# Performance work log

Measured on AMD Instinct MI355X. Metric: run time of the kernel, lower is better.

## Reference

```python
import jax, jax.numpy as jnp
import numpy as np

B, T, C = 1, 2048, 1024
H, HKV, DH, WIN = 16, 4, 64, 128
EPS = 1e-5


def rotate_half(x):
    x1, x2 = jnp.split(x, 2, axis=-1)
    return jnp.concatenate((-x2, x1), axis=-1)


def setup_inputs() -> dict:
    key = jax.random.key(0)
    ks = jax.random.split(key, 8)
    s = 0.02
    return {
        "x": jax.random.normal(ks[0], (B, T, C), dtype=jnp.float32),
        "Wq": jax.random.normal(ks[1], (C, H * DH), dtype=jnp.float32) * s,
        "Wk": jax.random.normal(ks[2], (C, HKV * DH), dtype=jnp.float32) * s,
        "Wv": jax.random.normal(ks[3], (C, HKV * DH), dtype=jnp.float32) * s,
        "Wc": jax.random.normal(ks[4], (C, C), dtype=jnp.float32) * s,
        "Wg": jax.random.normal(ks[5], (C, H), dtype=jnp.float32) * s,
        "bg": jax.random.normal(ks[6], (H,), dtype=jnp.float32) * s,
        "rms_w": jnp.ones((C,), dtype=jnp.float32),
    }


def reference(x, Wq, Wk, Wv, Wc, Wg, bg, rms_w):
    n_rep = H // HKV
    # projections -> [B, heads, T, DH]
    q = (x @ Wq).reshape(B, T, H, DH).transpose(0, 2, 1, 3)
    k = (x @ Wk).reshape(B, T, HKV, DH).transpose(0, 2, 1, 3)
    v = (x @ Wv).reshape(B, T, HKV, DH).transpose(0, 2, 1, 3)
    # rotary embedding (freqs duplicated across the two halves)
    inv_freq = 1.0 / (10000.0 ** (jnp.arange(0, DH, 2, dtype=jnp.float32) / DH))
    freqs = jnp.arange(T, dtype=jnp.float32)[:, None] * inv_freq[None, :]
    emb = jnp.concatenate((freqs, freqs), axis=-1)  # [T, DH]
    cos, sin = jnp.cos(emb)[None, None], jnp.sin(emb)[None, None]
    q = q * cos + rotate_half(q) * sin
    k = k * cos + rotate_half(k) * sin
    # GQA: repeat kv heads (contiguous repeat matches torch expand+reshape)
    k = jnp.repeat(k, n_rep, axis=1)
    v = jnp.repeat(v, n_rep, axis=1)
    # gated decay
    gate_logits = (x @ Wg + bg).reshape(B, T, H, 1).transpose(0, 2, 1, 3)  # [B,H,T,1]
    log_alpha = jax.nn.log_sigmoid(gate_logits)
    log_in_scale = jax.nn.log_sigmoid(-gate_logits)
    k_scaled = k * jnp.exp(log_in_scale)
    la_cum = jnp.cumsum(log_alpha, axis=2)                  # [B,H,T,1]
    log_decay = la_cum - jnp.swapaxes(la_cum, 2, 3)         # [B,H,T,T]
    causal = jnp.triu(jnp.ones((T, T), dtype=bool), k=1)
    decay = jnp.exp(jnp.where(causal, -jnp.inf, log_decay))
    scores = jnp.einsum('bhtd,bhsd->bhts', q, k_scaled)
    y_global = jnp.einsum('bhts,bhsd->bhtd', scores * decay, v)
    nb = T // WIN
    qb = q.reshape(B, H, nb, WIN, DH)
    kb = k.reshape(B, H, nb, WIN, DH)
    vb = v.reshape(B, H, nb, WIN, DH)
    att = jnp.einsum('bhnqd,bhnkd->bhnqk', qb, kb) / jnp.sqrt(jnp.float32(DH))
    wmask = jnp.triu(jnp.ones((WIN, WIN), dtype=bool), k=1)
    att = jax.nn.softmax(jnp.where(wmask, -jnp.inf, att), axis=-1)
    y_local = jnp.einsum('bhnqk,bhnkd->bhnqd', att, vb).reshape(B, H, T, DH)
    # fuse, RMSNorm, output projection
    y = (y_global + y_local).transpose(0, 2, 1, 3).reshape(B, T, C)
    y = y * jax.lax.rsqrt(jnp.mean(y * y, axis=-1, keepdims=True) + EPS) * rms_w
    return y @ Wc
```

## Files before the change

kernel.cpp:

```cpp
#include <hip/hip_runtime.h>
#include <hip/hip_bf16.h>


typedef __attribute__((ext_vector_type(8))) short bf16x8;
typedef __attribute__((ext_vector_type(4))) float f32x4;

#define MFMA16(a, b, c) __builtin_amdgcn_mfma_f32_16x16x32_bf16(a, b, c, 0, 0, 0)
#define LN10000_OVER_32 0.28782313662425575f

__device__ __forceinline__ short f2b(float f) {
  __hip_bfloat16 h = __float2bfloat16(f);
  return *reinterpret_cast<short*>(&h);
}
__device__ __forceinline__ float b2f(short s) {
  return __uint_as_float(((unsigned)(unsigned short)s) << 16);
}
__device__ __forceinline__ void gload16(const void* g, void* l) {
  __builtin_amdgcn_global_load_lds(
      (const __attribute__((address_space(1))) void*)g,
      (__attribute__((address_space(3))) void*)l, 16, 0, 0);
}

__device__ __forceinline__ void transpose_cvt_body(
    const float* __restrict__ src, short* __restrict__ dst, int R, int C,
    int bx, int by, float* ts , const float* __restrict__ sw) {
  int c0 = bx * 32, r0 = by * 32;
  int tr = threadIdx.x >> 3, tc = (threadIdx.x & 7) * 4;
  float4 v = *(const float4*)&src[(size_t)(r0 + tr) * C + c0 + tc];
  ts[tr * 33 + tc] = v.x;
  ts[tr * 33 + tc + 1] = v.y;
  ts[tr * 33 + tc + 2] = v.z;
  ts[tr * 33 + tc + 3] = v.w;
  __syncthreads();
  alignas(8) short o[4];
#pragma unroll
  for (int i = 0; i < 4; ++i) {
    float m = sw ? sw[r0 + tc + i] : 1.0f;
    o[i] = f2b(ts[(tc + i) * 33 + tr] * m);
  }
  *(uint2*)&dst[(size_t)(c0 + tr) * R + r0 + tc] = *(uint2*)o;
}

__global__ __launch_bounds__(256) void prep_fused(
    const float* __restrict__ x, const float* __restrict__ Wq,
    const float* __restrict__ Wk, const float* __restrict__ Wv,
    const float* __restrict__ Wc, const float* __restrict__ Wg,
    const float* __restrict__ bg, const float* __restrict__ rmsw,
    short* __restrict__ xb, short* __restrict__ wqkvT,
    short* __restrict__ wcT, float* __restrict__ g, float* __restrict__ rs) {
  __shared__ float ts[32 * 33];
  const int j = blockIdx.x;
  const int tid = threadIdx.x;
  if (j < 2048) {
    const int t = j;
    const int h = tid & 15, chunk = tid >> 4;
    const float* xr = x + (size_t)t * 1024 + chunk * 64;
    const float* wg = Wg + (size_t)chunk * 64 * 16 + h;
    float acc = 0.f;
#pragma unroll
    for (int c = 0; c < 64; c += 4) {
      float4 xv = *(const float4*)(xr + c);
      acc = fmaf(xv.x, wg[(c + 0) * 16], acc);
      acc = fmaf(xv.y, wg[(c + 1) * 16], acc);
      acc = fmaf(xv.z, wg[(c + 2) * 16], acc);
      acc = fmaf(xv.w, wg[(c + 3) * 16], acc);
    }
    ts[chunk * 16 + h] = acc;
    __syncthreads();
    if (tid < 16) {
      float s = bg[tid];
#pragma unroll
      for (int i = 0; i < 16; ++i) s += ts[i * 16 + tid];
      g[t * 16 + tid] = s;
    }
  } else if (j < 3072) {
    int i = ((j - 2048) * 256 + tid) * 8;
    float4 a = *(const float4*)(x + i);
    float4 b = *(const float4*)(x + i + 4);
    alignas(16) short o[8] = {f2b(a.x), f2b(a.y), f2b(a.z), f2b(a.w),
                              f2b(b.x), f2b(b.y), f2b(b.z), f2b(b.w)};
    *(float4*)(xb + i) = *(float4*)o;
  } else if (j < 4096) {
    int jj = j - 3072;
    transpose_cvt_body(Wq, wqkvT, 1024, 1024, jj & 31, jj >> 5, ts, nullptr);
  } else if (j < 4352) {
    int jj = j - 4096;
    transpose_cvt_body(Wk, wqkvT + 1024 * 1024, 1024, 256, jj & 7, jj >> 3, ts,
                       nullptr);
  } else if (j < 4608) {
    int jj = j - 4352;
    transpose_cvt_body(Wv, wqkvT + 1280 * 1024, 1024, 256, jj & 7, jj >> 3, ts,
                       nullptr);
  } else if (j < 5632) {
    int jj = j - 4608;
    transpose_cvt_body(Wc, wcT, 1024, 1024, jj & 31, jj >> 5, ts, rmsw);
  } else {
    int i4 = ((j - 5632) * 256 + tid) * 4;
    float4 z = {0.f, 0.f, 0.f, 0.f};
    *(float4*)(rs + i4) = z;
  }
}

__global__ __launch_bounds__(256) void qkv_gemm_fused(
    const short* __restrict__ A, const short* __restrict__ Bt,
    short* __restrict__ qkvb, short* __restrict__ vtb,
    short* __restrict__ ktb, const float* __restrict__ g,
    float* __restrict__ lac, float* __restrict__ insc) {
  __shared__ short As[128 * 64];
  __shared__ short Bs[64 * 64];
  __shared__ float part[256];
  const int id = blockIdx.x;
  const int tid = threadIdx.x;
  if (id >= 384) {
    const int h = id - 384;
    float vals[8];
    float local = 0.f;
#pragma unroll
    for (int i = 0; i < 8; ++i) {
      int t = tid * 8 + i;
      float gv = g[t * 16 + h];
      float la = (gv > 0.f) ? -log1pf(expf(-gv)) : (gv - log1pf(expf(gv)));
      insc[h * 2048 + t] = 1.f / (1.f + expf(gv));
      vals[i] = la;
      local += la;
    }
    part[tid] = local;
    __syncthreads();
    for (int off = 1; off < 256; off <<= 1) {
      float add = (tid >= off) ? part[tid - off] : 0.f;
      __syncthreads();
      part[tid] += add;
      __syncthreads();
    }
    float run = (tid > 0) ? part[tid - 1] : 0.f;
#pragma unroll
    for (int i = 0; i < 8; ++i) {
      run += vals[i];
      lac[h * 2048 + tid * 8 + i] = run;
    }
    return;
  }
  const int lane = tid & 63, wid = tid >> 6;
  const int l15 = lane & 15, lq = lane >> 4;
  const int jlin = id >> 3;
  const int by = (id & 7) + 8 * (jlin / 24);
  const int bx = jlin % 24;
  const int m0 = by * 128, n0 = bx * 64;
  const int K = 1024;
  const int srow = lane >> 3;
  const int sc16 = (lane & 7) ^ srow;
  f32x4 acc[2][4];
#pragma unroll
  for (int mt = 0; mt < 2; ++mt)
#pragma unroll
    for (int nt = 0; nt < 4; ++nt) acc[mt][nt] = {0.f, 0.f, 0.f, 0.f};
  for (int kt = 0; kt < K; kt += 64) {
    __syncthreads();
#pragma unroll
    for (int i = 0; i < 4; ++i) {
      int jj = wid * 4 + i;
      int row = jj * 8 + srow;
      gload16(A + (size_t)(m0 + row) * K + kt + sc16 * 8, &As[jj * 512]);
    }
#pragma unroll
    for (int i = 0; i < 2; ++i) {
      int jj = wid * 2 + i;
      int row = jj * 8 + srow;
      gload16(Bt + (size_t)(n0 + row) * K + kt + sc16 * 8, &Bs[jj * 512]);
    }
    __syncthreads();
    bf16x8 af[2][2], bfr[4][2];
#pragma unroll
    for (int ks = 0; ks < 2; ++ks) {
      int c16 = ks * 4 + lq;
#pragma unroll
      for (int mt = 0; mt < 2; ++mt) {
        int ar = wid * 32 + mt * 16 + l15;
        af[mt][ks] = *(const bf16x8*)&As[(ar * 8 + (c16 ^ (ar & 7))) * 8];
      }
#pragma unroll
      for (int nt = 0; nt < 4; ++nt) {
        int br = nt * 16 + l15;
        bfr[nt][ks] = *(const bf16x8*)&Bs[(br * 8 + (c16 ^ (br & 7))) * 8];
      }
    }
#pragma unroll
    for (int ks = 0; ks < 2; ++ks)
#pragma unroll
      for (int mt = 0; mt < 2; ++mt)
#pragma unroll
        for (int nt = 0; nt < 4; ++nt)
          acc[mt][nt] = MFMA16(af[mt][ks], bfr[nt][ks], acc[mt][nt]);
  }
  if (bx >= 20) {
#pragma unroll
    for (int mt = 0; mt < 2; ++mt) {
      int row0 = m0 + wid * 32 + mt * 16 + lq * 4;
#pragma unroll
      for (int nt = 0; nt < 4; ++nt) {
        int vcol = (n0 - 1280) + nt * 16 + l15;
        alignas(8) short o4[4];
#pragma unroll
        for (int r = 0; r < 4; ++r) o4[r] = f2b(acc[mt][nt][r]);
        *(uint2*)&vtb[(size_t)vcol * 2048 + row0] = *(uint2*)o4;
      }
    }
    return;
  }
  const bool isk = (bx >= 16);
#pragma unroll
  for (int mt = 0; mt < 2; ++mt) {
    int row0 = m0 + wid * 32 + mt * 16 + lq * 4;
#pragma unroll
    for (int nt = 0; nt < 2; ++nt) {
      int d = nt * 16 + l15;
      float ivf = __expf(-LN10000_OVER_32 * (float)d);
      alignas(8) short oa[4], ob[4];
#pragma unroll
      for (int r = 0; r < 4; ++r) {
        int row_g = row0 + r;
        float th = (float)row_g * ivf;
        float cs = cosf(th), sn = sinf(th);
        float a = acc[mt][nt][r], b = acc[mt][nt + 2][r];
        oa[r] = f2b(a * cs - b * sn);
        ob[r] = f2b(b * cs + a * sn);
        qkvb[(size_t)row_g * 1536 + n0 + d] = oa[r];
        qkvb[(size_t)row_g * 1536 + n0 + d + 32] = ob[r];
      }
      if (isk) {
        int dk = n0 - 1024 + d;
        *(uint2*)&ktb[(size_t)dk * 2048 + row0] = *(uint2*)oa;
        *(uint2*)&ktb[(size_t)(dk + 32) * 2048 + row0] = *(uint2*)ob;
      }
    }
  }
}

__global__ __launch_bounds__(256) void chunk_state(
    const short* __restrict__ vtb, const short* __restrict__ ktb,
    const float* __restrict__ lac, const float* __restrict__ insc,
    float* __restrict__ Bmat) {
  __shared__ short Ks[64 * 64], Vts[64 * 64];
  __shared__ float lacs[64], inss[64], gvals[64];
  const int tid = threadIdx.x, lane = tid & 63, wid = tid >> 6;
  const int l15 = lane & 15, lq = lane >> 4;
  const int h = blockIdx.y, kh = h >> 2, c = blockIdx.x;
  const int srow = lane >> 3;
  const int sc16 = (lane & 7) ^ srow;
#pragma unroll
  for (int i = 0; i < 2; ++i) {
    int jj = wid * 2 + i;
    int row = jj * 8 + srow;
    gload16(ktb + (size_t)(kh * 64 + row) * 2048 + c * 64 + sc16 * 8,
            &Ks[jj * 512]);
    gload16(vtb + (size_t)(kh * 64 + row) * 2048 + c * 64 + sc16 * 8,
            &Vts[jj * 512]);
  }
  if (tid < 64) {
    lacs[tid] = lac[h * 2048 + c * 64 + tid];
    inss[tid] = insc[h * 2048 + c * 64 + tid];
  }
  __syncthreads();
  if (tid < 64)
    gvals[tid] = __expf(fminf(lacs[63] - lacs[tid], 0.f)) * inss[tid];
  __syncthreads();
  const int er = wid * 16 + l15;
  bf16x8 av[2];
#pragma unroll
  for (int ks = 0; ks < 2; ++ks) {
    int c16 = ks * 4 + lq;
    bf16x8 raw = *(const bf16x8*)&Vts[(er * 8 + (c16 ^ (er & 7))) * 8];
    float4 g0 = *(const float4*)&gvals[c16 * 8];
    float4 g1 = *(const float4*)&gvals[c16 * 8 + 4];
    float gv[8] = {g0.x, g0.y, g0.z, g0.w, g1.x, g1.y, g1.z, g1.w};
    bf16x8 sc;
#pragma unroll
    for (int jx = 0; jx < 8; ++jx) sc[jx] = f2b(b2f(raw[jx]) * gv[jx]);
    av[ks] = sc;
  }
  f32x4 acc[4];
#pragma unroll
  for (int nt = 0; nt < 4; ++nt) acc[nt] = {0.f, 0.f, 0.f, 0.f};
#pragma unroll
  for (int ks = 0; ks < 2; ++ks) {
    int c16 = ks * 4 + lq;
#pragma unroll
    for (int nt = 0; nt < 4; ++nt) {
      int dr = nt * 16 + l15;
      bf16x8 bk = *(const bf16x8*)&Ks[(dr * 8 + (c16 ^ (dr & 7))) * 8];
      acc[nt] = MFMA16(av[ks], bk, acc[nt]);
    }
  }
  float* Bout = Bmat + (size_t)(h * 32 + c) * 4096;
#pragma unroll
  for (int nt = 0; nt < 4; ++nt)
#pragma unroll
    for (int r = 0; r < 4; ++r) {
      int e = wid * 16 + lq * 4 + r;
      Bout[e * 64 + nt * 16 + l15] = acc[nt][r];
    }
}

__global__ __launch_bounds__(256) void scan_kernel(
    const float* __restrict__ Bmat, const float* __restrict__ lac,
    short* __restrict__ St) {
  const int h = blockIdx.x, sl = blockIdx.y, tid = threadIdx.x;
  __shared__ float lacE[32];
  if (tid < 32) lacE[tid] = lac[h * 2048 + tid * 64 + 63];
  __syncthreads();
  const int base = sl * 512 + tid * 2;
  float S0 = 0.f, S1 = 0.f;
  *(unsigned*)&St[(size_t)(h * 32) * 4096 + base] = 0u;
  float2 p = *(const float2*)(Bmat + (size_t)(h * 32) * 4096 + base);
  for (int c = 1; c < 32; ++c) {
    float2 n = p;
    if (c < 31) n = *(const float2*)(Bmat + (size_t)(h * 32 + c) * 4096 + base);
    float a = (c >= 2) ? __expf(fminf(lacE[c - 1] - lacE[c - 2], 0.f)) : 0.f;
    S0 = fmaf(a, S0, p.x);
    S1 = fmaf(a, S1, p.y);
    unsigned pack = (unsigned)(unsigned short)f2b(S0) |
                    ((unsigned)(unsigned short)f2b(S1) << 16);
    *(unsigned*)&St[(size_t)(h * 32 + c) * 4096 + base] = pack;
    p = n;
  }
}

__global__ __launch_bounds__(256) void fused_attn(
    const short* __restrict__ qkv, const short* __restrict__ vtb,
    const short* __restrict__ St, const float* __restrict__ lac,
    const float* __restrict__ insc, short* __restrict__ ys,
    float* __restrict__ rs) {
  const int c = blockIdx.x, h = blockIdx.y;
  const int kh = h >> 2;
  const bool odd = (c & 1) != 0;
  __shared__ short Qs[64 * 64], Kd[64 * 64], Vd[64 * 64], Sts[64 * 64],
      Kp[64 * 64], Vp[64 * 64], Pd[64 * 64], Pp[64 * 64];
  __shared__ float lacq[64], inss[64];
  __shared__ float laprev_sh;
  const int tid = threadIdx.x, lane = tid & 63, wid = tid >> 6;
  const int l15 = lane & 15, lq = lane >> 4;
  const int srow = lane >> 3;
  const int sc16 = (lane & 7) ^ srow;
#pragma unroll
  for (int i = 0; i < 2; ++i) {
    int jj = wid * 2 + i;
    int row = jj * 8 + srow;
    gload16(qkv + (size_t)(c * 64 + row) * 1536 + h * 64 + sc16 * 8,
            &Qs[jj * 512]);
    gload16(qkv + (size_t)(c * 64 + row) * 1536 + 1024 + kh * 64 + sc16 * 8,
            &Kd[jj * 512]);
    gload16(vtb + (size_t)(kh * 64 + row) * 2048 + c * 64 + sc16 * 8,
            &Vd[jj * 512]);
    gload16(St + (size_t)(h * 32 + c) * 4096 + row * 64 + sc16 * 8,
            &Sts[jj * 512]);
  }
  if (odd) {
#pragma unroll
    for (int i = 0; i < 2; ++i) {
      int jj = wid * 2 + i;
      int row = jj * 8 + srow;
      gload16(qkv + (size_t)((c - 1) * 64 + row) * 1536 + 1024 + kh * 64 +
                  sc16 * 8,
              &Kp[jj * 512]);
      gload16(vtb + (size_t)(kh * 64 + row) * 2048 + (c - 1) * 64 + sc16 * 8,
              &Vp[jj * 512]);
    }
  }
  if (tid < 64) {
    lacq[tid] = lac[h * 2048 + c * 64 + tid];
    inss[tid] = insc[h * 2048 + c * 64 + tid];
  }
  if (tid == 0) laprev_sh = (c > 0) ? lac[h * 2048 + c * 64 - 1] : 1e30f;
  __syncthreads();
  const int qr = wid * 16 + l15;
  bf16x8 aq[2];
#pragma unroll
  for (int ks = 0; ks < 2; ++ks) {
    int c16 = ks * 4 + lq;
    aq[ks] = *(const bf16x8*)&Qs[(qr * 8 + (c16 ^ (qr & 7))) * 8];
  }
  f32x4 sv[4];
#pragma unroll
  for (int nt = 0; nt < 4; ++nt) {
    int kr = nt * 16 + l15;
    bf16x8 bk0 = *(const bf16x8*)&Kd[(kr * 8 + ((0 + lq) ^ (kr & 7))) * 8];
    bf16x8 bk1 = *(const bf16x8*)&Kd[(kr * 8 + ((4 + lq) ^ (kr & 7))) * 8];
    f32x4 z = {0.f, 0.f, 0.f, 0.f};
    z = MFMA16(aq[0], bk0, z);
    z = MFMA16(aq[1], bk1, z);
    sv[nt] = z;
  }
  f32x4 sp[4];
  if (odd) {
#pragma unroll
    for (int nt = 0; nt < 4; ++nt) {
      int kr = nt * 16 + l15;
      bf16x8 bk0 = *(const bf16x8*)&Kp[(kr * 8 + ((0 + lq) ^ (kr & 7))) * 8];
      bf16x8 bk1 = *(const bf16x8*)&Kp[(kr * 8 + ((4 + lq) ^ (kr & 7))) * 8];
      f32x4 z = {0.f, 0.f, 0.f, 0.f};
      z = MFMA16(aq[0], bk0, z);
      z = MFMA16(aq[1], bk1, z);
      sp[nt] = z;
    }
  } else {
#pragma unroll
    for (int nt = 0; nt < 4; ++nt) sp[nt] = {0.f, 0.f, 0.f, 0.f};
  }
  f32x4 oi[4];
#pragma unroll
  for (int nt = 0; nt < 4; ++nt) {
    int er = nt * 16 + l15;
    bf16x8 bs0 = *(const bf16x8*)&Sts[(er * 8 + ((0 + lq) ^ (er & 7))) * 8];
    bf16x8 bs1 = *(const bf16x8*)&Sts[(er * 8 + ((4 + lq) ^ (er & 7))) * 8];
    f32x4 z = {0.f, 0.f, 0.f, 0.f};
    z = MFMA16(aq[0], bs0, z);
    z = MFMA16(aq[1], bs1, z);
    oi[nt] = z;
  }
  float mrow[4], ssum[4];
  float vd[4][4], vp[4][4];
#pragma unroll
  for (int r = 0; r < 4; ++r) mrow[r] = -1e30f;
#pragma unroll
  for (int nt = 0; nt < 4; ++nt) {
    int col = nt * 16 + l15;
#pragma unroll
    for (int r = 0; r < 4; ++r) {
      int row = wid * 16 + lq * 4 + r;
      float xv = (col <= row) ? sv[nt][r] * 0.125f : -1e30f;
      vd[nt][r] = xv;
      mrow[r] = fmaxf(mrow[r], xv);
      if (odd) {
        float xp = sp[nt][r] * 0.125f;
        vp[nt][r] = xp;
        mrow[r] = fmaxf(mrow[r], xp);
      }
    }
  }
#pragma unroll
  for (int r = 0; r < 4; ++r) {
    for (int off = 1; off < 16; off <<= 1)
      mrow[r] = fmaxf(mrow[r], __shfl_xor(mrow[r], off, 64));
    ssum[r] = 0.f;
  }
#pragma unroll
  for (int nt = 0; nt < 4; ++nt) {
#pragma unroll
    for (int r = 0; r < 4; ++r) {
      float e = __expf(vd[nt][r] - mrow[r]);
      vd[nt][r] = e;
      ssum[r] += e;
      if (odd) {
        float ep = __expf(vp[nt][r] - mrow[r]);
        vp[nt][r] = ep;
        ssum[r] += ep;
      }
    }
  }
#pragma unroll
  for (int r = 0; r < 4; ++r) {
    for (int off = 1; off < 16; off <<= 1) ssum[r] += __shfl_xor(ssum[r], off, 64);
    ssum[r] = 1.f / ssum[r];
  }
#pragma unroll
  for (int nt = 0; nt < 4; ++nt) {
    int col = nt * 16 + l15;
    float ls = lacq[col], is = inss[col];
#pragma unroll
    for (int r = 0; r < 4; ++r) {
      int row = wid * 16 + lq * 4 + r;
      float w = __expf(fminf(lacq[row] - ls, 0.f)) * is;
      if (col > row) w = 0.f;
      float pc = sv[nt][r] * w + vd[nt][r] * ssum[r];
      Pd[(row * 8 + ((col >> 3) ^ (row & 7))) * 8 + (col & 7)] = f2b(pc);
      if (odd)
        Pp[(row * 8 + ((col >> 3) ^ (row & 7))) * 8 + (col & 7)] =
            f2b(vp[nt][r] * ssum[r]);
    }
  }
  __syncthreads();
  bf16x8 ap[2];
#pragma unroll
  for (int ks = 0; ks < 2; ++ks) {
    int c16 = ks * 4 + lq;
    ap[ks] = *(const bf16x8*)&Pd[(qr * 8 + (c16 ^ (qr & 7))) * 8];
  }
  f32x4 o[4];
#pragma unroll
  for (int nt = 0; nt < 4; ++nt) {
    int vr = nt * 16 + l15;
    bf16x8 bv0 = *(const bf16x8*)&Vd[(vr * 8 + ((0 + lq) ^ (vr & 7))) * 8];
    bf16x8 bv1 = *(const bf16x8*)&Vd[(vr * 8 + ((4 + lq) ^ (vr & 7))) * 8];
    f32x4 z = {0.f, 0.f, 0.f, 0.f};
    z = MFMA16(ap[0], bv0, z);
    z = MFMA16(ap[1], bv1, z);
    o[nt] = z;
  }
  if (odd) {
    bf16x8 app[2];
#pragma unroll
    for (int ks = 0; ks < 2; ++ks) {
      int c16 = ks * 4 + lq;
      app[ks] = *(const bf16x8*)&Pp[(qr * 8 + (c16 ^ (qr & 7))) * 8];
    }
#pragma unroll
    for (int nt = 0; nt < 4; ++nt) {
      int vr = nt * 16 + l15;
      bf16x8 bv0 = *(const bf16x8*)&Vp[(vr * 8 + ((0 + lq) ^ (vr & 7))) * 8];
      bf16x8 bv1 = *(const bf16x8*)&Vp[(vr * 8 + ((4 + lq) ^ (vr & 7))) * 8];
      o[nt] = MFMA16(app[0], bv0, o[nt]);
      o[nt] = MFMA16(app[1], bv1, o[nt]);
    }
  }
  const float laprev = laprev_sh;
#pragma unroll
  for (int r = 0; r < 4; ++r) {
    int row = wid * 16 + lq * 4 + r;
    float rfac = __expf(fminf(lacq[row] - laprev, 0.f));
    int row_g = c * 64 + row;
    float ssq = 0.f;
#pragma unroll
    for (int nt = 0; nt < 4; ++nt) {
      int colg = h * 64 + nt * 16 + l15;
      size_t idx = (size_t)row_g * 1024 + colg;
      float v = o[nt][r] + rfac * oi[nt][r];
      ys[idx] = f2b(v);
      ssq = fmaf(v, v, ssq);
    }
    for (int off = 1; off < 16; off <<= 1) ssq += __shfl_xor(ssq, off, 64);
    if (l15 == 0) atomicAdd(&rs[row_g], ssq);
  }
}

__global__ __launch_bounds__(256) void out_gemm(
    const short* __restrict__ A, const short* __restrict__ Bt,
    const float* __restrict__ rs, float* __restrict__ C) {
  __shared__ short As[64 * 64];
  __shared__ short Bs[64 * 64];
  const int tid = threadIdx.x, lane = tid & 63, wid = tid >> 6;
  const int l15 = lane & 15, lq = lane >> 4;
  const int wm = wid >> 1, wn = wid & 1;
  const int id = blockIdx.x;
  const int jlin = id >> 3;
  const int by = (id & 7) + 8 * (jlin / 16);
  const int bx = jlin % 16;
  const int m0 = by * 64, n0 = bx * 64;
  const int K = 1024;
  const int srow = lane >> 3;
  const int sc16 = (lane & 7) ^ srow;
  f32x4 acc[2][2];
#pragma unroll
  for (int mt = 0; mt < 2; ++mt)
#pragma unroll
    for (int nt = 0; nt < 2; ++nt) acc[mt][nt] = {0.f, 0.f, 0.f, 0.f};
  for (int kt = 0; kt < K; kt += 64) {
    __syncthreads();
#pragma unroll
    for (int i = 0; i < 2; ++i) {
      int jj = wid * 2 + i;
      int row = jj * 8 + srow;
      gload16(A + (size_t)(m0 + row) * K + kt + sc16 * 8, &As[jj * 512]);
      gload16(Bt + (size_t)(n0 + row) * K + kt + sc16 * 8, &Bs[jj * 512]);
    }
    __syncthreads();
    bf16x8 af[2][2], bfr[2][2];
#pragma unroll
    for (int ks = 0; ks < 2; ++ks) {
      int c16 = ks * 4 + lq;
#pragma unroll
      for (int mt = 0; mt < 2; ++mt) {
        int ar = wm * 32 + mt * 16 + l15;
        af[mt][ks] = *(const bf16x8*)&As[(ar * 8 + (c16 ^ (ar & 7))) * 8];
      }
#pragma unroll
      for (int nt = 0; nt < 2; ++nt) {
        int br = wn * 32 + nt * 16 + l15;
        bfr[nt][ks] = *(const bf16x8*)&Bs[(br * 8 + (c16 ^ (br & 7))) * 8];
      }
    }
#pragma unroll
    for (int ks = 0; ks < 2; ++ks)
#pragma unroll
      for (int mt = 0; mt < 2; ++mt)
#pragma unroll
        for (int nt = 0; nt < 2; ++nt)
          acc[mt][nt] = MFMA16(af[mt][ks], bfr[nt][ks], acc[mt][nt]);
  }
#pragma unroll
  for (int mt = 0; mt < 2; ++mt) {
    int row0 = m0 + wm * 32 + mt * 16 + lq * 4;
#pragma unroll
    for (int r = 0; r < 4; ++r) {
      int row_g = row0 + r;
      float sc = rsqrtf(rs[row_g] * (1.0f / 1024.0f) + 1e-5f);
#pragma unroll
      for (int nt = 0; nt < 2; ++nt)
        C[(size_t)row_g * 1024 + n0 + wn * 32 + nt * 16 + l15] =
            acc[mt][nt][r] * sc;
    }
  }
}

extern "C" void kernel_launch(void* const* d_in, const int* in_sizes, int n_in,
                              void* d_out, int out_size, void* d_ws,
                              size_t ws_size, hipStream_t stream) {
  const float* x = (const float*)d_in[0];
  const float* Wq = (const float*)d_in[1];
  const float* Wk = (const float*)d_in[2];
  const float* Wv = (const float*)d_in[3];
  const float* Wc = (const float*)d_in[4];
  const float* Wg = (const float*)d_in[5];
  const float* bg = (const float*)d_in[6];
  const float* rmsw = (const float*)d_in[7];
  float* out = (float*)d_out;

  short* wqkvT = (short*)d_ws;
  short* wcT = wqkvT + 1536 * 1024;
  short* qkvb = wcT + 1024 * 1024;
  short* vtb = qkvb + 2048 * 1536;
  short* ktb = vtb + 256 * 2048;
  float* gw = (float*)(ktb + 256 * 2048);
  float* lacw = gw + 2048 * 16;
  float* inscw = lacw + 16 * 2048;
  float* Bmat = inscw + 16 * 2048;
  short* Stb = (short*)(Bmat + 16 * 32 * 4096);
  short* xb = Stb + 16 * 32 * 4096;
  short* ys = xb;
  short* ylc = xb + 2048 * 1024;
  float* rsq = (float*)(ylc + 2048 * 1024);

  prep_fused<<<5634, 256, 0, stream>>>(x, Wq, Wk, Wv, Wc, Wg, bg, rmsw, xb,
                                       wqkvT, wcT, gw, rsq);
  qkv_gemm_fused<<<400, 256, 0, stream>>>(xb, wqkvT, qkvb, vtb, ktb, gw, lacw,
                                          inscw);
  chunk_state<<<dim3(32, 16), 256, 0, stream>>>(vtb, ktb, lacw, inscw, Bmat);
  scan_kernel<<<dim3(16, 8), 256, 0, stream>>>(Bmat, lacw, Stb);
  fused_attn<<<dim3(32, 16), 256, 0, stream>>>(qkvb, vtb, Stb, lacw, inscw,
                                               ys, rsq);
  out_gemm<<<512, 256, 0, stream>>>(ys, wcT, rsq, out);
}
```

Baseline: 133.7 us.

## Fuse chunk-state, scan, attention and output GEMM into one cooperative kernel

Replaces four separate back-end launches (chunk_state, scan, fused_attn, out_gemm) with a single cooperative kernel of 512 blocks that uses grid-wide syncs between phases and reuses one shared-memory buffer across phases. The aim is to remove kernel launch gaps and tail effects between small dependent kernels. In exchange it needs all 512 blocks co-resident, forces launch_bounds occupancy of 2 blocks per unit with 64KB of shared memory, and leaves most blocks idle during the scan phase.

New measurement: 326.5 us. 144% more time.

```diff
diff --git a/kernel.cpp b/kernel.cpp
--- a/kernel.cpp
+++ b/kernel.cpp
@@ -1,5 +1,8 @@
 #include <hip/hip_runtime.h>
 #include <hip/hip_bf16.h>
+#include <hip/hip_cooperative_groups.h>
+
+namespace cg = cooperative_groups;
 
 
 typedef __attribute__((ext_vector_type(8))) short bf16x8;
@@ -236,367 +239,374 @@
   }
 }
 
-__global__ __launch_bounds__(256) void chunk_state(
-    const short* __restrict__ vtb, const short* __restrict__ ktb,
-    const float* __restrict__ lac, const float* __restrict__ insc,
-    float* __restrict__ Bmat) {
-  __shared__ short Ks[64 * 64], Vts[64 * 64];
-  __shared__ float lacs[64], inss[64], gvals[64];
-  const int tid = threadIdx.x, lane = tid & 63, wid = tid >> 6;
-  const int l15 = lane & 15, lq = lane >> 4;
-  const int h = blockIdx.y, kh = h >> 2, c = blockIdx.x;
-  const int srow = lane >> 3;
-  const int sc16 = (lane & 7) ^ srow;
-#pragma unroll
-  for (int i = 0; i < 2; ++i) {
-    int jj = wid * 2 + i;
-    int row = jj * 8 + srow;
-    gload16(ktb + (size_t)(kh * 64 + row) * 2048 + c * 64 + sc16 * 8,
-            &Ks[jj * 512]);
-    gload16(vtb + (size_t)(kh * 64 + row) * 2048 + c * 64 + sc16 * 8,
-            &Vts[jj * 512]);
-  }
-  if (tid < 64) {
-    lacs[tid] = lac[h * 2048 + c * 64 + tid];
-    inss[tid] = insc[h * 2048 + c * 64 + tid];
-  }
-  __syncthreads();
-  if (tid < 64)
-    gvals[tid] = __expf(fminf(lacs[63] - lacs[tid], 0.f)) * inss[tid];
-  __syncthreads();
-  const int er = wid * 16 + l15;
-  bf16x8 av[2];
-#pragma unroll
-  for (int ks = 0; ks < 2; ++ks) {
-    int c16 = ks * 4 + lq;
-    bf16x8 raw = *(const bf16x8*)&Vts[(er * 8 + (c16 ^ (er & 7))) * 8];
-    float4 g0 = *(const float4*)&gvals[c16 * 8];
-    float4 g1 = *(const float4*)&gvals[c16 * 8 + 4];
-    float gv[8] = {g0.x, g0.y, g0.z, g0.w, g1.x, g1.y, g1.z, g1.w};
-    bf16x8 sc;
-#pragma unroll
-    for (int jx = 0; jx < 8; ++jx) sc[jx] = f2b(b2f(raw[jx]) * gv[jx]);
-    av[ks] = sc;
-  }
-  f32x4 acc[4];
-#pragma unroll
-  for (int nt = 0; nt < 4; ++nt) acc[nt] = {0.f, 0.f, 0.f, 0.f};
-#pragma unroll
-  for (int ks = 0; ks < 2; ++ks) {
-    int c16 = ks * 4 + lq;
-#pragma unroll
-    for (int nt = 0; nt < 4; ++nt) {
-      int dr = nt * 16 + l15;
-      bf16x8 bk = *(const bf16x8*)&Ks[(dr * 8 + (c16 ^ (dr & 7))) * 8];
-      acc[nt] = MFMA16(av[ks], bk, acc[nt]);
-    }
-  }
-  float* Bout = Bmat + (size_t)(h * 32 + c) * 4096;
-#pragma unroll
-  for (int nt = 0; nt < 4; ++nt)
-#pragma unroll
-    for (int r = 0; r < 4; ++r) {
-      int e = wid * 16 + lq * 4 + r;
-      Bout[e * 64 + nt * 16 + l15] = acc[nt][r];
-    }
-}
-
-__global__ __launch_bounds__(256) void scan_kernel(
-    const float* __restrict__ Bmat, const float* __restrict__ lac,
-    short* __restrict__ St) {
-  const int h = blockIdx.x, sl = blockIdx.y, tid = threadIdx.x;
-  __shared__ float lacE[32];
-  if (tid < 32) lacE[tid] = lac[h * 2048 + tid * 64 + 63];
-  __syncthreads();
-  const int base = sl * 512 + tid * 2;
-  float S0 = 0.f, S1 = 0.f;
-  *(unsigned*)&St[(size_t)(h * 32) * 4096 + base] = 0u;
-  float2 p = *(const float2*)(Bmat + (size_t)(h * 32) * 4096 + base);
-  for (int c = 1; c < 32; ++c) {
-    float2 n = p;
-    if (c < 31) n = *(const float2*)(Bmat + (size_t)(h * 32 + c) * 4096 + base);
-    float a = (c >= 2) ? __expf(fminf(lacE[c - 1] - lacE[c - 2], 0.f)) : 0.f;
-    S0 = fmaf(a, S0, p.x);
-    S1 = fmaf(a, S1, p.y);
-    unsigned pack = (unsigned)(unsigned short)f2b(S0) |
-                    ((unsigned)(unsigned short)f2b(S1) << 16);
-    *(unsigned*)&St[(size_t)(h * 32 + c) * 4096 + base] = pack;
-    p = n;
-  }
-}
-
-__global__ __launch_bounds__(256) void fused_attn(
+__global__ __launch_bounds__(256, 2) void mega_back(
     const short* __restrict__ qkv, const short* __restrict__ vtb,
-    const short* __restrict__ St, const float* __restrict__ lac,
-    const float* __restrict__ insc, short* __restrict__ ys,
-    float* __restrict__ rs) {
-  const int c = blockIdx.x, h = blockIdx.y;
-  const int kh = h >> 2;
-  const bool odd = (c & 1) != 0;
-  __shared__ short Qs[64 * 64], Kd[64 * 64], Vd[64 * 64], Sts[64 * 64],
-      Kp[64 * 64], Vp[64 * 64], Pd[64 * 64], Pp[64 * 64];
-  __shared__ float lacq[64], inss[64];
+    const short* __restrict__ ktb, const float* __restrict__ lac,
+    const float* __restrict__ insc, float* __restrict__ Bmat,
+    short* __restrict__ St, short* __restrict__ ys, float* __restrict__ rs,
+    const short* __restrict__ wcT, float* __restrict__ out) {
+  __shared__ short smem[8 * 4096];
+  __shared__ float fbuf[3 * 64];
   __shared__ float laprev_sh;
+  cg::grid_group grid = cg::this_grid();
+
+  const int bid = blockIdx.x;
   const int tid = threadIdx.x, lane = tid & 63, wid = tid >> 6;
   const int l15 = lane & 15, lq = lane >> 4;
   const int srow = lane >> 3;
   const int sc16 = (lane & 7) ^ srow;
-#pragma unroll
-  for (int i = 0; i < 2; ++i) {
-    int jj = wid * 2 + i;
-    int row = jj * 8 + srow;
-    gload16(qkv + (size_t)(c * 64 + row) * 1536 + h * 64 + sc16 * 8,
-            &Qs[jj * 512]);
-    gload16(qkv + (size_t)(c * 64 + row) * 1536 + 1024 + kh * 64 + sc16 * 8,
-            &Kd[jj * 512]);
-    gload16(vtb + (size_t)(kh * 64 + row) * 2048 + c * 64 + sc16 * 8,
-            &Vd[jj * 512]);
-    gload16(St + (size_t)(h * 32 + c) * 4096 + row * 64 + sc16 * 8,
-            &Sts[jj * 512]);
-  }
-  if (odd) {
+
+  {
+    const int c = bid & 31, h = bid >> 5, kh = h >> 2;
+    short* Ks = smem;
+    short* Vts = smem + 4096;
+    float* lacs = fbuf;
+    float* inss = fbuf + 64;
+    float* gvals = fbuf + 128;
 #pragma unroll
     for (int i = 0; i < 2; ++i) {
       int jj = wid * 2 + i;
       int row = jj * 8 + srow;
-      gload16(qkv + (size_t)((c - 1) * 64 + row) * 1536 + 1024 + kh * 64 +
-                  sc16 * 8,
-              &Kp[jj * 512]);
-      gload16(vtb + (size_t)(kh * 64 + row) * 2048 + (c - 1) * 64 + sc16 * 8,
-              &Vp[jj * 512]);
-    }
-  }
-  if (tid < 64) {
-    lacq[tid] = lac[h * 2048 + c * 64 + tid];
-    inss[tid] = insc[h * 2048 + c * 64 + tid];
-  }
-  if (tid == 0) laprev_sh = (c > 0) ? lac[h * 2048 + c * 64 - 1] : 1e30f;
-  __syncthreads();
-  const int qr = wid * 16 + l15;
-  bf16x8 aq[2];
-#pragma unroll
-  for (int ks = 0; ks < 2; ++ks) {
-    int c16 = ks * 4 + lq;
-    aq[ks] = *(const bf16x8*)&Qs[(qr * 8 + (c16 ^ (qr & 7))) * 8];
-  }
-  f32x4 sv[4];
-#pragma unroll
-  for (int nt = 0; nt < 4; ++nt) {
-    int kr = nt * 16 + l15;
-    bf16x8 bk0 = *(const bf16x8*)&Kd[(kr * 8 + ((0 + lq) ^ (kr & 7))) * 8];
-    bf16x8 bk1 = *(const bf16x8*)&Kd[(kr * 8 + ((4 + lq) ^ (kr & 7))) * 8];
-    f32x4 z = {0.f, 0.f, 0.f, 0.f};
-    z = MFMA16(aq[0], bk0, z);
-    z = MFMA16(aq[1], bk1, z);
-    sv[nt] = z;
-  }
-  f32x4 sp[4];
-  if (odd) {
+      gload16(ktb + (size_t)(kh * 64 + row) * 2048 + c * 64 + sc16 * 8,
+              &Ks[jj * 512]);
+      gload16(vtb + (size_t)(kh * 64 + row) * 2048 + c * 64 + sc16 * 8,
+              &Vts[jj * 512]);
+    }
+    if (tid < 64) {
+      lacs[tid] = lac[h * 2048 + c * 64 + tid];
+      inss[tid] = insc[h * 2048 + c * 64 + tid];
+    }
+    __syncthreads();
+    if (tid < 64)
+      gvals[tid] = __expf(fminf(lacs[63] - lacs[tid], 0.f)) * inss[tid];
+    __syncthreads();
+    const int er = wid * 16 + l15;
+    bf16x8 av[2];
+#pragma unroll
+    for (int ks = 0; ks < 2; ++ks) {
+      int c16 = ks * 4 + lq;
+      bf16x8 raw = *(const bf16x8*)&Vts[(er * 8 + (c16 ^ (er & 7))) * 8];
+      float4 g0 = *(const float4*)&gvals[c16 * 8];
+      float4 g1 = *(const float4*)&gvals[c16 * 8 + 4];
+      float gv[8] = {g0.x, g0.y, g0.z, g0.w, g1.x, g1.y, g1.z, g1.w};
+      bf16x8 sc;
+#pragma unroll
+      for (int jx = 0; jx < 8; ++jx) sc[jx] = f2b(b2f(raw[jx]) * gv[jx]);
+      av[ks] = sc;
+    }
+    f32x4 acc[4];
+#pragma unroll
+    for (int nt = 0; nt < 4; ++nt) acc[nt] = {0.f, 0.f, 0.f, 0.f};
+#pragma unroll
+    for (int ks = 0; ks < 2; ++ks) {
+      int c16 = ks * 4 + lq;
+#pragma unroll
+      for (int nt = 0; nt < 4; ++nt) {
+        int dr = nt * 16 + l15;
+        bf16x8 bk = *(const bf16x8*)&Ks[(dr * 8 + (c16 ^ (dr & 7))) * 8];
+        acc[nt] = MFMA16(av[ks], bk, acc[nt]);
+      }
+    }
+    float* Bout = Bmat + (size_t)(h * 32 + c) * 4096;
+#pragma unroll
+    for (int nt = 0; nt < 4; ++nt)
+#pragma unroll
+      for (int r = 0; r < 4; ++r) {
+        int e = wid * 16 + lq * 4 + r;
+        Bout[e * 64 + nt * 16 + l15] = acc[nt][r];
+      }
+  }
+  grid.sync();
+
+  if (bid < 128) {
+    const int h = bid >> 3, sl = bid & 7;
+    float* lacE = fbuf + 128;
+    if (tid < 32) lacE[tid] = lac[h * 2048 + tid * 64 + 63];
+    __syncthreads();
+    const int base = sl * 512 + tid * 2;
+    float S0 = 0.f, S1 = 0.f;
+    *(unsigned*)&St[(size_t)(h * 32) * 4096 + base] = 0u;
+    float2 p = *(const float2*)(Bmat + (size_t)(h * 32) * 4096 + base);
+    for (int c = 1; c < 32; ++c) {
+      float2 n = p;
+      if (c < 31)
+        n = *(const float2*)(Bmat + (size_t)(h * 32 + c) * 4096 + base);
+      float a = (c >= 2) ? __expf(fminf(lacE[c - 1] - lacE[c - 2], 0.f)) : 0.f;
+      S0 = fmaf(a, S0, p.x);
+      S1 = fmaf(a, S1, p.y);
+      unsigned pack = (unsigned)(unsigned short)f2b(S0) |
+                      ((unsigned)(unsigned short)f2b(S1) << 16);
+      *(unsigned*)&St[(size_t)(h * 32 + c) * 4096 + base] = pack;
+      p = n;
+    }
+  }
+  grid.sync();
+
+  {
+    const int c = bid & 31, h = bid >> 5, kh = h >> 2;
+    const bool odd = (c & 1) != 0;
+    short* Qs = smem;
+    short* Kd = smem + 4096;
+    short* Vd = smem + 2 * 4096;
+    short* Sts = smem + 3 * 4096;
+    short* Kp = smem + 4 * 4096;
+    short* Vp = smem + 5 * 4096;
+    short* Pd = smem + 6 * 4096;
+    short* Pp = smem + 7 * 4096;
+    float* lacq = fbuf;
+    float* inss = fbuf + 64;
+#pragma unroll
+    for (int i = 0; i < 2; ++i) {
+      int jj = wid * 2 + i;
+      int row = jj * 8 + srow;
+      gload16(qkv + (size_t)(c * 64 + row) * 1536 + h * 64 + sc16 * 8,
+              &Qs[jj * 512]);
+      gload16(qkv + (size_t)(c * 64 + row) * 1536 + 1024 + kh * 64 + sc16 * 8,
+              &Kd[jj * 512]);
+      gload16(vtb + (size_t)(kh * 64 + row) * 2048 + c * 64 + sc16 * 8,
+              &Vd[jj * 512]);
+      gload16(St + (size_t)(h * 32 + c) * 4096 + row * 64 + sc16 * 8,
+              &Sts[jj * 512]);
+    }
+    if (odd) {
+#pragma unroll
+      for (int i = 0; i < 2; ++i) {
+        int jj = wid * 2 + i;
+        int row = jj * 8 + srow;
+        gload16(qkv + (size_t)((c - 1) * 64 + row) * 1536 + 1024 + kh * 64 +
+                    sc16 * 8,
+                &Kp[jj * 512]);
+        gload16(vtb + (size_t)(kh * 64 + row) * 2048 + (c - 1) * 64 + sc16 * 8,
+                &Vp[jj * 512]);
+      }
+    }
+    if (tid < 64) {
+      lacq[tid] = lac[h * 2048 + c * 64 + tid];
+      inss[tid] = insc[h * 2048 + c * 64 + tid];
+    }
+    if (tid == 0) laprev_sh = (c > 0) ? lac[h * 2048 + c * 64 - 1] : 1e30f;
+    __syncthreads();
+    const int qr = wid * 16 + l15;
+    bf16x8 aq[2];
+#pragma unroll
+    for (int ks = 0; ks < 2; ++ks) {
+      int c16 = ks * 4 + lq;
+      aq[ks] = *(const bf16x8*)&Qs[(qr * 8 + (c16 ^ (qr & 7))) * 8];
+    }
+    f32x4 sv[4];
 #pragma unroll
     for (int nt = 0; nt < 4; ++nt) {
       int kr = nt * 16 + l15;
-      bf16x8 bk0 = *(const bf16x8*)&Kp[(kr * 8 + ((0 + lq) ^ (kr & 7))) * 8];
-      bf16x8 bk1 = *(const bf16x8*)&Kp[(kr * 8 + ((4 + lq) ^ (kr & 7))) * 8];
+      bf16x8 bk0 = *(const bf16x8*)&Kd[(kr * 8 + ((0 + lq) ^ (kr & 7))) * 8];
+      bf16x8 bk1 = *(const bf16x8*)&Kd[(kr * 8 + ((4 + lq) ^ (kr & 7))) * 8];
       f32x4 z = {0.f, 0.f, 0.f, 0.f};
       z = MFMA16(aq[0], bk0, z);
       z = MFMA16(aq[1], bk1, z);
-      sp[nt] = z;
-    }
-  } else {
-#pragma unroll
-    for (int nt = 0; nt < 4; ++nt) sp[nt] = {0.f, 0.f, 0.f, 0.f};
-  }
-  f32x4 oi[4];
-#pragma unroll
-  for (int nt = 0; nt < 4; ++nt) {
-    int er = nt * 16 + l15;
-    bf16x8 bs0 = *(const bf16x8*)&Sts[(er * 8 + ((0 + lq) ^ (er & 7))) * 8];
-    bf16x8 bs1 = *(const bf16x8*)&Sts[(er * 8 + ((4 + lq) ^ (er & 7))) * 8];
-    f32x4 z = {0.f, 0.f, 0.f, 0.f};
-    z = MFMA16(aq[0], bs0, z);
-    z = MFMA16(aq[1], bs1, z);
-    oi[nt] = z;
-  }
-  float mrow[4], ssum[4];
-  float vd[4][4], vp[4][4];
-#pragma unroll
-  for (int r = 0; r < 4; ++r) mrow[r] = -1e30f;
-#pragma unroll
-  for (int nt = 0; nt < 4; ++nt) {
-    int col = nt * 16 + l15;
+      sv[nt] = z;
+    }
+    f32x4 sp[4];
+    if (odd) {
+#pragma unroll
+      for (int nt = 0; nt < 4; ++nt) {
+        int kr = nt * 16 + l15;
+        bf16x8 bk0 = *(const bf16x8*)&Kp[(kr * 8 + ((0 + lq) ^ (kr & 7))) * 8];
+        bf16x8 bk1 = *(const bf16x8*)&Kp[(kr * 8 + ((4 + lq) ^ (kr & 7))) * 8];
+        f32x4 z = {0.f, 0.f, 0.f, 0.f};
+        z = MFMA16(aq[0], bk0, z);
+        z = MFMA16(aq[1], bk1, z);
+        sp[nt] = z;
+      }
+    } else {
+#pragma unroll
+      for (int nt = 0; nt < 4; ++nt) sp[nt] = {0.f, 0.f, 0.f, 0.f};
+    }
+    f32x4 oi[4];
+#pragma unroll
+    for (int nt = 0; nt < 4; ++nt) {
+      int er = nt * 16 + l15;
+      bf16x8 bs0 = *(const bf16x8*)&Sts[(er * 8 + ((0 + lq) ^ (er & 7))) * 8];
+      bf16x8 bs1 = *(const bf16x8*)&Sts[(er * 8 + ((4 + lq) ^ (er & 7))) * 8];
+      f32x4 z = {0.f, 0.f, 0.f, 0.f};
+      z = MFMA16(aq[0], bs0, z);
+      z = MFMA16(aq[1], bs1, z);
+      oi[nt] = z;
+    }
+    float mrow[4], ssum[4];
+    float vd[4][4], vp[4][4];
+#pragma unroll
+    for (int r = 0; r < 4; ++r) mrow[r] = -1e30f;
+#pragma unroll
+    for (int nt = 0; nt < 4; ++nt) {
+      int col = nt * 16 + l15;
+#pragma unroll
+      for (int r = 0; r < 4; ++r) {
+        int row = wid * 16 + lq * 4 + r;
+        float xv = (col <= row) ? sv[nt][r] * 0.125f : -1e30f;
+        vd[nt][r] = xv;
+        mrow[r] = fmaxf(mrow[r], xv);
+        if (odd) {
+          float xp = sp[nt][r] * 0.125f;
+          vp[nt][r] = xp;
+          mrow[r] = fmaxf(mrow[r], xp);
+        }
+      }
+    }
+#pragma unroll
+    for (int r = 0; r < 4; ++r) {
+      for (int off = 1; off < 16; off <<= 1)
+        mrow[r] = fmaxf(mrow[r], __shfl_xor(mrow[r], off, 64));
+      ssum[r] = 0.f;
+    }
+#pragma unroll
+    for (int nt = 0; nt < 4; ++nt) {
+#pragma unroll
+      for (int r = 0; r < 4; ++r) {
+        float e = __expf(vd[nt][r] - mrow[r]);
+        vd[nt][r] = e;
+        ssum[r] += e;
+        if (odd) {
+          float ep = __expf(vp[nt][r] - mrow[r]);
+          vp[nt][r] = ep;
+          ssum[r] += ep;
+        }
+      }
+    }
+#pragma unroll
+    for (int r = 0; r < 4; ++r) {
+      for (int off = 1; off < 16; off <<= 1)
+        ssum[r] += __shfl_xor(ssum[r], off, 64);
+      ssum[r] = 1.f / ssum[r];
+    }
+#pragma unroll
+    for (int nt = 0; nt < 4; ++nt) {
+      int col = nt * 16 + l15;
+      float ls = lacq[col], is = inss[col];
+#pragma unroll
+      for (int r = 0; r < 4; ++r) {
+        int row = wid * 16 + lq * 4 + r;
+        float w = __expf(fminf(lacq[row] - ls, 0.f)) * is;
+        if (col > row) w = 0.f;
+        float pc = sv[nt][r] * w + vd[nt][r] * ssum[r];
+        Pd[(row * 8 + ((col >> 3) ^ (row & 7))) * 8 + (col & 7)] = f2b(pc);
+        if (odd)
+          Pp[(row * 8 + ((col >> 3) ^ (row & 7))) * 8 + (col & 7)] =
+              f2b(vp[nt][r] * ssum[r]);
+      }
+    }
+    __syncthreads();
+    bf16x8 ap[2];
+#pragma unroll
+    for (int ks = 0; ks < 2; ++ks) {
+      int c16 = ks * 4 + lq;
+      ap[ks] = *(const bf16x8*)&Pd[(qr * 8 + (c16 ^ (qr & 7))) * 8];
+    }
+    f32x4 o[4];
+#pragma unroll
+    for (int nt = 0; nt < 4; ++nt) {
+      int vr = nt * 16 + l15;
+      bf16x8 bv0 = *(const bf16x8*)&Vd[(vr * 8 + ((0 + lq) ^ (vr & 7))) * 8];
+      bf16x8 bv1 = *(const bf16x8*)&Vd[(vr * 8 + ((4 + lq) ^ (vr & 7))) * 8];
+      f32x4 z = {0.f, 0.f, 0.f, 0.f};
+      z = MFMA16(ap[0], bv0, z);
+      z = MFMA16(ap[1], bv1, z);
+      o[nt] = z;
+    }
+    if (odd) {
+      bf16x8 app[2];
+#pragma unroll
+      for (int ks = 0; ks < 2; ++ks) {
+        int c16 = ks * 4 + lq;
+        app[ks] = *(const bf16x8*)&Pp[(qr * 8 + (c16 ^ (qr & 7))) * 8];
+      }
+#pragma unroll
+      for (int nt = 0; nt < 4; ++nt) {
+        int vr = nt * 16 + l15;
+        bf16x8 bv0 = *(const bf16x8*)&Vp[(vr * 8 + ((0 + lq) ^ (vr & 7))) * 8];
+        bf16x8 bv1 = *(const bf16x8*)&Vp[(vr * 8 + ((4 + lq) ^ (vr & 7))) * 8];
+        o[nt] = MFMA16(app[0], bv0, o[nt]);
+        o[nt] = MFMA16(app[1], bv1, o[nt]);
+      }
+    }
+    const float laprev = laprev_sh;
 #pragma unroll
     for (int r = 0; r < 4; ++r) {
       int row = wid * 16 + lq * 4 + r;
-      float xv = (col <= row) ? sv[nt][r] * 0.125f : -1e30f;
-      vd[nt][r] = xv;
-      mrow[r] = fmaxf(mrow[r], xv);
-      if (odd) {
-        float xp = sp[nt][r] * 0.125f;
-        vp[nt][r] = xp;
-        mrow[r] = fmaxf(mrow[r], xp);
-      }
-    }
-  }
-#pragma unroll
-  for (int r = 0; r < 4; ++r) {
-    for (int off = 1; off < 16; off <<= 1)
-      mrow[r] = fmaxf(mrow[r], __shfl_xor(mrow[r], off, 64));
-    ssum[r] = 0.f;
-  }
-#pragma unroll
-  for (int nt = 0; nt < 4; ++nt) {
-#pragma unroll
-    for (int r = 0; r < 4; ++r) {
-      float e = __expf(vd[nt][r] - mrow[r]);
-      vd[nt][r] = e;
-      ssum[r] += e;
-      if (odd) {
-        float ep = __expf(vp[nt][r] - mrow[r]);
-        vp[nt][r] = ep;
-        ssum[r] += ep;
-      }
-    }
-  }
-#pragma unroll
-  for (int r = 0; r < 4; ++r) {
-    for (int off = 1; off < 16; off <<= 1) ssum[r] += __shfl_xor(ssum[r], off, 64);
-    ssum[r] = 1.f / ssum[r];
-  }
-#pragma unroll
-  for (int nt = 0; nt < 4; ++nt) {
-    int col = nt * 16 + l15;
-    float ls = lacq[col], is = inss[col];
-#pragma unroll
-    for (int r = 0; r < 4; ++r) {
-      int row = wid * 16 + lq * 4 + r;
-      float w = __expf(fminf(lacq[row] - ls, 0.f)) * is;
-      if (col > row) w = 0.f;
-      float pc = sv[nt][r] * w + vd[nt][r] * ssum[r];
-      Pd[(row * 8 + ((col >> 3) ^ (row & 7))) * 8 + (col & 7)] = f2b(pc);
-      if (odd)
-        Pp[(row * 8 + ((col >> 3) ^ (row & 7))) * 8 + (col & 7)] =
-            f2b(vp[nt][r] * ssum[r]);
-    }
-  }
-  __syncthreads();
-  bf16x8 ap[2];
-#pragma unroll
-  for (int ks = 0; ks < 2; ++ks) {
-    int c16 = ks * 4 + lq;
-    ap[ks] = *(const bf16x8*)&Pd[(qr * 8 + (c16 ^ (qr & 7))) * 8];
-  }
-  f32x4 o[4];
-#pragma unroll
-  for (int nt = 0; nt < 4; ++nt) {
-    int vr = nt * 16 + l15;
-    bf16x8 bv0 = *(const bf16x8*)&Vd[(vr * 8 + ((0 + lq) ^ (vr & 7))) * 8];
-    bf16x8 bv1 = *(const bf16x8*)&Vd[(vr * 8 + ((4 + lq) ^ (vr & 7))) * 8];
-    f32x4 z = {0.f, 0.f, 0.f, 0.f};
-    z = MFMA16(ap[0], bv0, z);
-    z = MFMA16(ap[1], bv1, z);
-    o[nt] = z;
-  }
-  if (odd) {
-    bf16x8 app[2];
-#pragma unroll
-    for (int ks = 0; ks < 2; ++ks) {
-      int c16 = ks * 4 + lq;
-      app[ks] = *(const bf16x8*)&Pp[(qr * 8 + (c16 ^ (qr & 7))) * 8];
-    }
-#pragma unroll
-    for (int nt = 0; nt < 4; ++nt) {
-      int vr = nt * 16 + l15;
-      bf16x8 bv0 = *(const bf16x8*)&Vp[(vr * 8 + ((0 + lq) ^ (vr & 7))) * 8];
-      bf16x8 bv1 = *(const bf16x8*)&Vp[(vr * 8 + ((4 + lq) ^ (vr & 7))) * 8];
-      o[nt] = MFMA16(app[0], bv0, o[nt]);
-      o[nt] = MFMA16(app[1], bv1, o[nt]);
-    }
-  }
-  const float laprev = laprev_sh;
-#pragma unroll
-  for (int r = 0; r < 4; ++r) {
-    int row = wid * 16 + lq * 4 + r;
-    float rfac = __expf(fminf(lacq[row] - laprev, 0.f));
-    int row_g = c * 64 + row;
-    float ssq = 0.f;
-#pragma unroll
-    for (int nt = 0; nt < 4; ++nt) {
-      int colg = h * 64 + nt * 16 + l15;
-      size_t idx = (size_t)row_g * 1024 + colg;
-      float v = o[nt][r] + rfac * oi[nt][r];
-      ys[idx] = f2b(v);
-      ssq = fmaf(v, v, ssq);
-    }
-    for (int off = 1; off < 16; off <<= 1) ssq += __shfl_xor(ssq, off, 64);
-    if (l15 == 0) atomicAdd(&rs[row_g], ssq);
-  }
-}
-
-__global__ __launch_bounds__(256) void out_gemm(
-    const short* __restrict__ A, const short* __restrict__ Bt,
-    const float* __restrict__ rs, float* __restrict__ C) {
-  __shared__ short As[64 * 64];
-  __shared__ short Bs[64 * 64];
-  const int tid = threadIdx.x, lane = tid & 63, wid = tid >> 6;
-  const int l15 = lane & 15, lq = lane >> 4;
-  const int wm = wid >> 1, wn = wid & 1;
-  const int id = blockIdx.x;
-  const int jlin = id >> 3;
-  const int by = (id & 7) + 8 * (jlin / 16);
-  const int bx = jlin % 16;
-  const int m0 = by * 64, n0 = bx * 64;
-  const int K = 1024;
-  const int srow = lane >> 3;
-  const int sc16 = (lane & 7) ^ srow;
-  f32x4 acc[2][2];
-#pragma unroll
-  for (int mt = 0; mt < 2; ++mt)
-#pragma unroll
-    for (int nt = 0; nt < 2; ++nt) acc[mt][nt] = {0.f, 0.f, 0.f, 0.f};
-  for (int kt = 0; kt < K; kt += 64) {
-    __syncthreads();
-#pragma unroll
-    for (int i = 0; i < 2; ++i) {
-      int jj = wid * 2 + i;
-      int row = jj * 8 + srow;
-      gload16(A + (size_t)(m0 + row) * K + kt + sc16 * 8, &As[jj * 512]);
-      gload16(Bt + (size_t)(n0 + row) * K + kt + sc16 * 8, &Bs[jj * 512]);
-    }
-    __syncthreads();
-    bf16x8 af[2][2], bfr[2][2];
-#pragma unroll
-    for (int ks = 0; ks < 2; ++ks) {
-      int c16 = ks * 4 + lq;
-#pragma unroll
-      for (int mt = 0; mt < 2; ++mt) {
-        int ar = wm * 32 + mt * 16 + l15;
-        af[mt][ks] = *(const bf16x8*)&As[(ar * 8 + (c16 ^ (ar & 7))) * 8];
-      }
-#pragma unroll
-      for (int nt = 0; nt < 2; ++nt) {
-        int br = wn * 32 + nt * 16 + l15;
-        bfr[nt][ks] = *(const bf16x8*)&Bs[(br * 8 + (c16 ^ (br & 7))) * 8];
-      }
-    }
-#pragma unroll
-    for (int ks = 0; ks < 2; ++ks)
-#pragma unroll
-      for (int mt = 0; mt < 2; ++mt)
+      float rfac = __expf(fminf(lacq[row] - laprev, 0.f));
+      int row_g = c * 64 + row;
+      float ssq = 0.f;
+#pragma unroll
+      for (int nt = 0; nt < 4; ++nt) {
+        int colg = h * 64 + nt * 16 + l15;
+        size_t idx = (size_t)row_g * 1024 + colg;
+        float v = o[nt][r] + rfac * oi[nt][r];
+        ys[idx] = f2b(v);
+        ssq = fmaf(v, v, ssq);
+      }
+      for (int off = 1; off < 16; off <<= 1) ssq += __shfl_xor(ssq, off, 64);
+      if (l15 == 0) atomicAdd(&rs[row_g], ssq);
+    }
+  }
+  grid.sync();
+
+  {
+    short* As = smem;
+    short* Bs = smem + 4096;
+    const int wm = wid >> 1, wn = wid & 1;
+    const int jlin = bid >> 3;
+    const int by = (bid & 7) + 8 * (jlin / 16);
+    const int bx = jlin % 16;
+    const int m0 = by * 64, n0 = bx * 64;
+    const int K = 1024;
+    f32x4 acc[2][2];
+#pragma unroll
+    for (int mt = 0; mt < 2; ++mt)
+#pragma unroll
+      for (int nt = 0; nt < 2; ++nt) acc[mt][nt] = {0.f, 0.f, 0.f, 0.f};
+    for (int kt = 0; kt < K; kt += 64) {
+      __syncthreads();
+#pragma unroll
+      for (int i = 0; i < 2; ++i) {
+        int jj = wid * 2 + i;
+        int row = jj * 8 + srow;
+        gload16(ys + (size_t)(m0 + row) * K + kt + sc16 * 8, &As[jj * 512]);
+        gload16(wcT + (size_t)(n0 + row) * K + kt + sc16 * 8, &Bs[jj * 512]);
+      }
+      __syncthreads();
+      bf16x8 af[2][2], bfr[2][2];
+#pragma unroll
+      for (int ks = 0; ks < 2; ++ks) {
+        int c16 = ks * 4 + lq;
+#pragma unroll
+        for (int mt = 0; mt < 2; ++mt) {
+          int ar = wm * 32 + mt * 16 + l15;
+          af[mt][ks] = *(const bf16x8*)&As[(ar * 8 + (c16 ^ (ar & 7))) * 8];
+        }
+#pragma unroll
+        for (int nt = 0; nt < 2; ++nt) {
+          int br = wn * 32 + nt * 16 + l15;
+          bfr[nt][ks] = *(const bf16x8*)&Bs[(br * 8 + (c16 ^ (br & 7))) * 8];
+        }
+      }
+#pragma unroll
+      for (int ks = 0; ks < 2; ++ks)
+#pragma unroll
+        for (int mt = 0; mt < 2; ++mt)
+#pragma unroll
+          for (int nt = 0; nt < 2; ++nt)
+            acc[mt][nt] = MFMA16(af[mt][ks], bfr[nt][ks], acc[mt][nt]);
+    }
+#pragma unroll
+    for (int mt = 0; mt < 2; ++mt) {
+      int row0 = m0 + wm * 32 + mt * 16 + lq * 4;
+#pragma unroll
+      for (int r = 0; r < 4; ++r) {
+        int row_g = row0 + r;
+        float sc = rsqrtf(rs[row_g] * (1.0f / 1024.0f) + 1e-5f);
 #pragma unroll
         for (int nt = 0; nt < 2; ++nt)
-          acc[mt][nt] = MFMA16(af[mt][ks], bfr[nt][ks], acc[mt][nt]);
-  }
-#pragma unroll
-  for (int mt = 0; mt < 2; ++mt) {
-    int row0 = m0 + wm * 32 + mt * 16 + lq * 4;
-#pragma unroll
-    for (int r = 0; r < 4; ++r) {
-      int row_g = row0 + r;
-      float sc = rsqrtf(rs[row_g] * (1.0f / 1024.0f) + 1e-5f);
-#pragma unroll
-      for (int nt = 0; nt < 2; ++nt)
-        C[(size_t)row_g * 1024 + n0 + wn * 32 + nt * 16 + l15] =
-            acc[mt][nt][r] * sc;
+          out[(size_t)row_g * 1024 + n0 + wn * 32 + nt * 16 + l15] =
+              acc[mt][nt][r] * sc;
+      }
     }
   }
 }
@@ -633,9 +643,16 @@
                                        wqkvT, wcT, gw, rsq);
   qkv_gemm_fused<<<400, 256, 0, stream>>>(xb, wqkvT, qkvb, vtb, ktb, gw, lacw,
                                           inscw);
-  chunk_state<<<dim3(32, 16), 256, 0, stream>>>(vtb, ktb, lacw, inscw, Bmat);
-  scan_kernel<<<dim3(16, 8), 256, 0, stream>>>(Bmat, lacw, Stb);
-  fused_attn<<<dim3(32, 16), 256, 0, stream>>>(qkvb, vtb, Stb, lacw, inscw,
-                                               ys, rsq);
-  out_gemm<<<512, 256, 0, stream>>>(ys, wcT, rsq, out);
-}
+  const short* qkvb_c = qkvb;
+  const short* vtb_c = vtb;
+  const short* ktb_c = ktb;
+  const float* lacw_c = lacw;
+  const float* inscw_c = inscw;
+  const short* wcT_c = wcT;
+  void* margs[] = {(void*)&qkvb_c, (void*)&vtb_c,  (void*)&ktb_c,
+                   (void*)&lacw_c, (void*)&inscw_c, (void*)&Bmat,
+                   (void*)&Stb,    (void*)&ys,      (void*)&rsq,
+                   (void*)&wcT_c,  (void*)&out};
+  hipLaunchCooperativeKernel((void*)mega_back, dim3(512), dim3(256), margs, 0,
+                             stream);
+}
```
